# Optimization experiments

Hardware: AMD Instinct MI355X
Metric: run time of the kernel (lower is better)

The kernel has to match this reference:

```python
import jax, jax.numpy as jnp
import numpy as np

N_QUBITS = 6
DIM = 2 ** N_QUBITS  # 64
Q_LAYERS = 2
CHUNK = 16

# ---- single-qubit rotation gate matrices (batched over leading dim) ----

def _rx(t):
    c = jnp.cos(t / 2).astype(jnp.complex64)
    s = jnp.sin(t / 2).astype(jnp.complex64)
    return jnp.stack([jnp.stack([c, -1j * s], -1), jnp.stack([-1j * s, c], -1)], -2)

def _ry(t):
    c = jnp.cos(t / 2).astype(jnp.complex64)
    s = jnp.sin(t / 2).astype(jnp.complex64)
    return jnp.stack([jnp.stack([c, -s], -1), jnp.stack([s, c], -1)], -2)

def _rz(t):
    e = jnp.exp(-0.5j * t.astype(jnp.complex64))
    z = jnp.zeros_like(e)
    return jnp.stack([jnp.stack([e, z], -1), jnp.stack([z, jnp.conj(e)], -1)], -2)


def _apply_1q(state, gate, wire):
    # state: (B, 64) complex64; gate: (B,2,2). PennyLane wire 0 = most-significant bit.
    dl, dr = 2 ** wire, 2 ** (N_QUBITS - 1 - wire)
    s = state.reshape(-1, dl, 2, dr)
    s = jnp.einsum('bkj,bljr->blkr', gate, s)
    return s.reshape(-1, DIM)


def _apply_crx(state, theta, control, target):
    s = state.reshape((-1,) + (2,) * N_QUBITS)
    s = jnp.moveaxis(s, (control + 1, target + 1), (1, 2))
    g = _rx(theta)  # (B,2,2)
    s1 = jnp.einsum('bkj,bj...->bk...', g, s[:, 1])
    s = jnp.concatenate([s[:, :1], s1[:, None]], axis=1)
    s = jnp.moveaxis(s, (1, 2), (control + 1, target + 1))
    return s.reshape(-1, DIM)


def _ansatz(state, params, n_layers):
    # unified ansatz: per layer, RX/RY/RZ on each qubit, ring of CRX forward, ring of CRX backward
    idx = 0
    for _ in range(n_layers):
        for i in range(N_QUBITS):
            state = _apply_1q(state, _rx(params[:, idx]), i)
            state = _apply_1q(state, _ry(params[:, idx + 1]), i)
            state = _apply_1q(state, _rz(params[:, idx + 2]), i)
            idx += 3
        for i in range(N_QUBITS):
            state = _apply_crx(state, params[:, idx], i, (i + 1) % N_QUBITS)
            idx += 1
        for i in range(N_QUBITS - 1, -1, -1):
            state = _apply_crx(state, params[:, idx], i, (i - 1) % N_QUBITS)
            idx += 1
    return state


_PX = jnp.array([[0, 1], [1, 0]], jnp.complex64)
_PY = jnp.array([[0, -1j], [1j, 0]], jnp.complex64)
_PZ = jnp.array([[1, 0], [0, -1]], jnp.complex64)


def _expvals(state):
    # expectations of X_i, Y_i, Z_i for all qubits -> (B, 3*n_qubits)
    outs = []
    B = state.shape[0]
    for P in (_PX, _PY, _PZ):
        g = jnp.broadcast_to(P, (B, 2, 2))
        for i in range(N_QUBITS):
            ps = _apply_1q(state, g, i)
            outs.append(jnp.sum(jnp.conj(state) * ps, axis=1).real)
    return jnp.stack(outs, axis=1).astype(jnp.float32)


def _forward(x, emb_w, emb_b, att_w1, att_b1, att_w2, att_b2, proj_w, proj_b,
             mix_re, mix_im, qff_params, out_w, out_b, ln_g, ln_b,
             cls_w1, cls_b1, cls_w2, cls_b2):
    B, C, T = x.shape
    # classical feature extractor: (B,C,T) -> (B,T,D)
    feats = jnp.einsum('bct,cd->btd', x, emb_w) + emb_b
    D = feats.shape[-1]
    n_chunks = T // CHUNK
    xc = feats.reshape(B, n_chunks, CHUNK, D)
    # attention-weighted chunk aggregation
    h = jnp.tanh(xc @ att_w1 + att_b1)
    scores = h @ att_w2 + att_b2                      # (B,nc,CHUNK,1)
    w = jax.nn.softmax(scores, axis=2)
    chunks = jnp.sum(w * xc, axis=2)                  # (B,nc,D)
    # quantum attention core: per-chunk ansatz params
    params = jax.nn.sigmoid(chunks @ proj_w + proj_b)  # (B,nc,60)
    flat = params.reshape(B * n_chunks, -1)
    state0 = jnp.zeros((B * n_chunks, DIM), jnp.complex64).at[:, 0].set(1.0)
    evolved = _ansatz(state0, flat, Q_LAYERS).reshape(B, n_chunks, DIM)
    # LCU mixing
    coeffs = (mix_re + 1j * mix_im).astype(jnp.complex64)
    coeffs = coeffs / (jnp.abs(coeffs).sum() + 1e-8)
    mixed = jnp.einsum('bti,t->bi', evolved, coeffs)
    norms = jnp.linalg.norm(mixed, axis=1, keepdims=True)
    mixed = mixed / (norms + 1e-9)
    # quantum feed-forward (shared params) + multi-observable measurement
    qp = jnp.broadcast_to(qff_params, (B, qff_params.shape[0]))
    qstate = _ansatz(mixed, qp, 1)
    qfeat = _expvals(qstate)                          # (B,18)
    out = qfeat @ out_w + out_b                       # (B,D)
    # LayerNorm
    mu = out.mean(-1, keepdims=True)
    var = out.var(-1, keepdims=True)
    out = (out - mu) / jnp.sqrt(var + 1e-5) * ln_g + ln_b
    # classifier head
    h2 = jax.nn.relu(out @ cls_w1 + cls_b1)
    return h2 @ cls_w2 + cls_b2


def setup_inputs() -> dict:
    key = jax.random.key(0)
    ks = jax.random.split(key, 20)
    B, C, T, D = 128, 64, 2048, 256
    NC = T // CHUNK        # 128 chunks
    NCP = 5 * N_QUBITS * Q_LAYERS  # 60 circuit params
    def nrm(k, shape, scale=0.05):
        return jax.random.normal(k, shape, jnp.float32) * scale
    return {
        'x': jax.random.normal(ks[0], (B, C, T), jnp.float32),
        'emb_w': nrm(ks[1], (C, D)), 'emb_b': nrm(ks[2], (D,)),
        'att_w1': nrm(ks[3], (D, D // 2)), 'att_b1': nrm(ks[4], (D // 2,)),
        'att_w2': nrm(ks[5], (D // 2, 1)), 'att_b2': nrm(ks[6], (1,)),
        'proj_w': nrm(ks[7], (D, NCP)), 'proj_b': nrm(ks[8], (NCP,)),
        'mix_re': jax.random.uniform(ks[9], (NC,), jnp.float32),
        'mix_im': jax.random.uniform(ks[10], (NC,), jnp.float32),
        'qff_params': nrm(ks[11], (5 * N_QUBITS,), 0.1),
        'out_w': nrm(ks[12], (3 * N_QUBITS, D)), 'out_b': nrm(ks[13], (D,)),
        'ln_g': jnp.ones((D,), jnp.float32), 'ln_b': jnp.zeros((D,), jnp.float32),
        'cls_w1': nrm(ks[14], (D, D)), 'cls_b1': nrm(ks[15], (D,)),
        'cls_w2': nrm(ks[16], (D, 2)), 'cls_b2': nrm(ks[17], (2,)),
    }


def reference(x, emb_w, emb_b, att_w1, att_b1, att_w2, att_b2, proj_w, proj_b,
              mix_re, mix_im, qff_params, out_w, out_b, ln_g, ln_b,
              cls_w1, cls_b1, cls_w2, cls_b2):
    return _forward(x, emb_w, emb_b, att_w1, att_b1, att_w2, att_b2, proj_w, proj_b,
                    mix_re, mix_im, qff_params, out_w, out_b, ln_g, ln_b,
                    cls_w1, cls_b1, cls_w2, cls_b2)
```

## Files before the change

### kernel.cpp

```cpp
#include <hip/hip_runtime.h>
#include <math.h>

#define NQ    6
#define QDIM  64
#define BB    128
#define CC    64
#define TT    2048
#define DD    256
#define NCH   128
#define CHLEN 16
#define HH    128
#define NCP   60

typedef __bf16 bf16x8 __attribute__((ext_vector_type(8)));
typedef float  f32x4  __attribute__((ext_vector_type(4)));

__device__ __forceinline__ unsigned short bfbits(__bf16 v) {
  return __builtin_bit_cast(unsigned short, v);
}

__device__ __forceinline__ float fast_tanh(float x) {
  float e = __expf(2.f * x);
  return 1.f - 2.f / (e + 1.f);
}

__device__ __forceinline__ float wave_sum(float v) {
#pragma unroll
  for (int off = 32; off >= 1; off >>= 1) v += __shfl_xor(v, off, 64);
  return v;
}

__device__ __forceinline__ void g_rx(float& re, float& im, int lane, int m, float half) {
  float c = __cosf(half), s = __sinf(half);
  float pre = __shfl_xor(re, m, 64);
  float pim = __shfl_xor(im, m, 64);
  float nre = c * re + s * pim;
  float nim = c * im - s * pre;
  re = nre; im = nim;
}
__device__ __forceinline__ void g_ry(float& re, float& im, int lane, int m, float half) {
  float c = __cosf(half), s = __sinf(half);
  float pre = __shfl_xor(re, m, 64);
  float pim = __shfl_xor(im, m, 64);
  float sg = (lane & m) ? s : -s;
  re = c * re + sg * pre;
  im = c * im + sg * pim;
}
__device__ __forceinline__ void g_rz(float& re, float& im, int lane, int m, float half) {
  float c = __cosf(half), s = __sinf(half);
  float sg = (lane & m) ? s : -s;
  float nre = c * re - sg * im;
  float nim = c * im + sg * re;
  re = nre; im = nim;
}
__device__ __forceinline__ void g_crx(float& re, float& im, int lane, int mc, int mt, float half) {
  float c = __cosf(half), s = __sinf(half);
  float pre = __shfl_xor(re, mt, 64);
  float pim = __shfl_xor(im, mt, 64);
  if (lane & mc) {
    float nre = c * re + s * pim;
    float nim = c * im - s * pre;
    re = nre; im = nim;
  }
}
__device__ __forceinline__ void ansatz_layer(float& re, float& im, int lane,
                                             const float* p) {
#pragma unroll
  for (int q = 0; q < 6; ++q) {
    int m = 1 << (5 - q);
    g_rx(re, im, lane, m, 0.5f * p[3 * q + 0]);
    g_ry(re, im, lane, m, 0.5f * p[3 * q + 1]);
    g_rz(re, im, lane, m, 0.5f * p[3 * q + 2]);
  }
#pragma unroll
  for (int q = 0; q < 6; ++q)
    g_crx(re, im, lane, 1 << (5 - q), 1 << (5 - ((q + 1) % 6)), 0.5f * p[18 + q]);
#pragma unroll
  for (int q = 5; q >= 0; --q)
    g_crx(re, im, lane, 1 << (5 - q), 1 << (5 - ((q + 5) % 6)), 0.5f * p[24 + (5 - q)]);
}

__global__ __launch_bounds__(256) void k0_prep(
    const float* __restrict__ emb_w, const float* __restrict__ emb_b,
    const float* __restrict__ att_w1, const float* __restrict__ att_b1,
    const float* __restrict__ proj_w, const float* __restrict__ proj_b,
    __bf16* __restrict__ WfH, __bf16* __restrict__ WfL,
    __bf16* __restrict__ PfH, __bf16* __restrict__ PfL,
    float* __restrict__ b_fused, float* __restrict__ pb_fused) {
  int idx = blockIdx.x * 256 + threadIdx.x;
  if (idx < 65536) {
    int out = idx >> 3, part = idx & 7;
    int j = out & 127, k = out >> 7;
    int d0 = part * 32;
    float a = 0.f;
#pragma unroll 8
    for (int d = d0; d < d0 + 32; ++d)
      a = fmaf(emb_w[k * 256 + d], att_w1[d * 128 + j], a);
    a += __shfl_xor(a, 1, 64); a += __shfl_xor(a, 2, 64); a += __shfl_xor(a, 4, 64);
    if (part == 0) {
      __bf16 h = (__bf16)a;
      WfH[j * 64 + k] = h; WfL[j * 64 + k] = (__bf16)(a - (float)h);
    }
  } else if (idx < 98304) {
    int i2 = idx - 65536;
    int out = i2 >> 3, part = i2 & 7;
    int n = out & 63, k = out >> 6;
    float a = 0.f;
    if (n < 60) {
      int d0 = part * 32;
#pragma unroll 8
      for (int d = d0; d < d0 + 32; ++d)
        a = fmaf(emb_w[k * 256 + d], proj_w[d * 60 + n], a);
    }
    a += __shfl_xor(a, 1, 64); a += __shfl_xor(a, 2, 64); a += __shfl_xor(a, 4, 64);
    if (part == 0) {
      __bf16 h = (__bf16)a;
      PfH[n * 64 + k] = h; PfL[n * 64 + k] = (__bf16)(a - (float)h);
    }
  } else if (idx < 99328) {
    int i3 = idx - 98304;
    int out = i3 >> 3, part = i3 & 7;
    float a = (part == 0) ? att_b1[out] : 0.f;
    int d0 = part * 32;
#pragma unroll 8
    for (int d = d0; d < d0 + 32; ++d)
      a = fmaf(emb_b[d], att_w1[d * 128 + out], a);
    a += __shfl_xor(a, 1, 64); a += __shfl_xor(a, 2, 64); a += __shfl_xor(a, 4, 64);
    if (part == 0) b_fused[out] = a;
  } else if (idx < 99840) {
    int i4 = idx - 99328;
    int out = i4 >> 3, part = i4 & 7;
    float a = 0.f;
    if (out < 60) {
      if (part == 0) a = proj_b[out];
      int d0 = part * 32;
#pragma unroll 8
      for (int d = d0; d < d0 + 32; ++d)
        a = fmaf(emb_b[d], proj_w[d * 60 + out], a);
    }
    a += __shfl_xor(a, 1, 64); a += __shfl_xor(a, 2, 64); a += __shfl_xor(a, 4, 64);
    if (part == 0) pb_fused[out] = a;
  }
}

__global__ __launch_bounds__(256, 8) void k1_fused(
    const float* __restrict__ x, const float* __restrict__ att_w2,
    const __bf16* __restrict__ WfH, const __bf16* __restrict__ WfL,
    const __bf16* __restrict__ PfH, const __bf16* __restrict__ PfL,
    const float* __restrict__ b_fused, const float* __restrict__ pb_fused,
    float2* __restrict__ evolved) {
  const int blk = blockIdx.x;
  const int b = blk >> 5, cq = blk & 31;
  const int tid = threadIdx.x, wv = tid >> 6, lane = tid & 63;
  const int l15 = lane & 15, quad = lane >> 4;

  __shared__ float4 uniF4[1024];
  __shared__ float scoreS[4][64];
  __shared__ float wSm[4][16];
  __shared__ __align__(16) __bf16 axH[4][64];
  __shared__ __align__(16) __bf16 axL[4][64];
  char* uni = (char*)uniF4;
  bf16x8* afH = (bf16x8*)uni;
  bf16x8* afL = (bf16x8*)(uni + 8192);
  float*  paramsS = (float*)uni;
  float4* matS    = (float4*)(uni + 960);
  float2* crxS    = (float2*)(uni + 4032);

  {
    unsigned short* afHu = (unsigned short*)uni;
    unsigned short* afLu = (unsigned short*)(uni + 8192);
#pragma unroll
    for (int p = 0; p < 2; ++p) {
      int slot = p * 256 + tid;
      int t4 = slot & 15, kp = slot >> 4;
      int k0 = kp * 2;
      const float* base = x + ((size_t)(b * 64 + k0)) * 2048 + cq * 64 + t4 * 4;
      float4 v0 = *(const float4*)base;
      float4 v1 = *(const float4*)(base + 2048);
      int ks = k0 >> 5, colq = (k0 >> 3) & 3, e = k0 & 7;
      float a0[4] = {v0.x, v0.y, v0.z, v0.w};
      float a1[4] = {v1.x, v1.y, v1.z, v1.w};
#pragma unroll
      for (int dt = 0; dt < 4; ++dt) {
        int t = t4 * 4 + dt;
        int frag = (t >> 4) * 2 + ks;
        int ln = (t & 15) + colq * 16;
        int widx = frag * 512 + ln * 8 + e;
        __bf16 h0 = (__bf16)a0[dt]; __bf16 l0 = (__bf16)(a0[dt] - (float)h0);
        __bf16 h1 = (__bf16)a1[dt]; __bf16 l1 = (__bf16)(a1[dt] - (float)h1);
        *(ushort2*)(afHu + widx) = make_ushort2(bfbits(h0), bfbits(h1));
        *(ushort2*)(afLu + widx) = make_ushort2(bfbits(l0), bfbits(l1));
      }
    }
  }
  __syncthreads();

  {
    float w2v[2], b1v[2];
#pragma unroll
    for (int jt = 0; jt < 2; ++jt) {
      int j = wv * 32 + jt * 16 + l15;
      w2v[jt] = att_w2[j];
      b1v[jt] = b_fused[j];
    }
#pragma unroll
    for (int half = 0; half < 2; ++half) {
      f32x4 acc[2][2];
#pragma unroll
      for (int a2 = 0; a2 < 2; ++a2)
#pragma unroll
        for (int c2 = 0; c2 < 2; ++c2) acc[a2][c2] = (f32x4){0.f, 0.f, 0.f, 0.f};
#pragma unroll
      for (int ks = 0; ks < 2; ++ks)
#pragma unroll
        for (int jt = 0; jt < 2; ++jt) {
          const size_t row = (size_t)(wv * 32 + jt * 16 + l15) * 64 + ks * 32 + 8 * quad;
          bf16x8 bh = *(const bf16x8*)(WfH + row);
          bf16x8 bl = *(const bf16x8*)(WfL + row);
#pragma unroll
          for (int mtl = 0; mtl < 2; ++mtl) {
            int frag = (half * 2 + mtl) * 2 + ks;
            bf16x8 ah = afH[frag * 64 + lane];
            bf16x8 al = afL[frag * 64 + lane];
            acc[mtl][jt] = __builtin_amdgcn_mfma_f32_16x16x32_bf16(ah, bh, acc[mtl][jt], 0, 0, 0);
            acc[mtl][jt] = __builtin_amdgcn_mfma_f32_16x16x32_bf16(al, bh, acc[mtl][jt], 0, 0, 0);
            acc[mtl][jt] = __builtin_amdgcn_mfma_f32_16x16x32_bf16(ah, bl, acc[mtl][jt], 0, 0, 0);
          }
        }
#pragma unroll
      for (int mtl = 0; mtl < 2; ++mtl)
#pragma unroll
        for (int r = 0; r < 4; ++r) {
          float sc = fast_tanh(acc[mtl][0][r] + b1v[0]) * w2v[0] +
                     fast_tanh(acc[mtl][1][r] + b1v[1]) * w2v[1];
          sc += __shfl_xor(sc, 1, 64);
          sc += __shfl_xor(sc, 2, 64);
          sc += __shfl_xor(sc, 4, 64);
          sc += __shfl_xor(sc, 8, 64);
          if (l15 == 0) scoreS[wv][(half * 2 + mtl) * 16 + quad * 4 + r] = sc;
        }
    }
  }
  __syncthreads();

  if (tid < 64) {
    const int c = tid >> 4, t = tid & 15, ct = c * 16 + t;
    float s = (scoreS[0][ct] + scoreS[1][ct]) + (scoreS[2][ct] + scoreS[3][ct]);
    float mx = s;
    mx = fmaxf(mx, __shfl_xor(mx, 1, 64));
    mx = fmaxf(mx, __shfl_xor(mx, 2, 64));
    mx = fmaxf(mx, __shfl_xor(mx, 4, 64));
    mx = fmaxf(mx, __shfl_xor(mx, 8, 64));
    float e = __expf(s - mx);
    float sum = e;
    sum += __shfl_xor(sum, 1, 64);
    sum += __shfl_xor(sum, 2, 64);
    sum += __shfl_xor(sum, 4, 64);
    sum += __shfl_xor(sum, 8, 64);
    wSm[c][t] = e / sum;
  }
  __syncthreads();

  {
    float wgt = wSm[wv][l15];
#pragma unroll
    for (int ks = 0; ks < 2; ++ks) {
      bf16x8 h8 = afH[(wv * 2 + ks) * 64 + lane];
      bf16x8 l8 = afL[(wv * 2 + ks) * 64 + lane];
      float part[8];
#pragma unroll
      for (int e = 0; e < 8; ++e) part[e] = wgt * ((float)h8[e] + (float)l8[e]);
#pragma unroll
      for (int off = 1; off <= 8; off <<= 1)
#pragma unroll
        for (int e = 0; e < 8; ++e) part[e] += __shfl_xor(part[e], off, 64);
      int kbase = ks * 32 + quad * 8;
      if (l15 == 0) {
        bf16x8 H;
#pragma unroll
        for (int e = 0; e < 8; ++e) H[e] = (__bf16)part[e];
        *(bf16x8*)(&axH[wv][kbase]) = H;
      } else if (l15 == 1) {
        bf16x8 L;
#pragma unroll
        for (int e = 0; e < 8; ++e) {
          __bf16 hh = (__bf16)part[e];
          L[e] = (__bf16)(part[e] - (float)hh);
        }
        *(bf16x8*)(&axL[wv][kbase]) = L;
      }
    }
  }
  __syncthreads();

  {
    const int jout = wv * 16 + l15;
    f32x4 acc3 = (f32x4){0.f, 0.f, 0.f, 0.f};
#pragma unroll
    for (int ks = 0; ks < 2; ++ks) {
      const size_t row = (size_t)jout * 64 + ks * 32 + 8 * quad;
      bf16x8 bh = *(const bf16x8*)(PfH + row);
      bf16x8 bl = *(const bf16x8*)(PfL + row);
      bf16x8 ax = (bf16x8)(__bf16)0.f, alx = (bf16x8)(__bf16)0.f;
      if (l15 < 4) {
        ax  = *(const bf16x8*)(&axH[0][0] + l15 * 64 + ks * 32 + 8 * quad);
        alx = *(const bf16x8*)(&axL[0][0] + l15 * 64 + ks * 32 + 8 * quad);
      }
      acc3 = __builtin_amdgcn_mfma_f32_16x16x32_bf16(ax, bh, acc3, 0, 0, 0);
      acc3 = __builtin_amdgcn_mfma_f32_16x16x32_bf16(alx, bh, acc3, 0, 0, 0);
      acc3 = __builtin_amdgcn_mfma_f32_16x16x32_bf16(ax, bl, acc3, 0, 0, 0);
    }
    if (jout < 60 && quad == 0) {
      float pbias = pb_fused[jout];
      const int layer = (jout >= 30) ? 1 : 0;
      const int pm = jout - layer * 30;
#pragma unroll
      for (int r = 0; r < 4; ++r) {
        float a = acc3[r] + pbias;
        float p = 1.f / (1.f + __expf(-a));
        paramsS[r * 60 + jout] = p;
        if (pm >= 18) {
          float sn, cs;
          __sincosf(0.5f * p, &sn, &cs);
          crxS[r * 24 + layer * 12 + (pm - 18)] = make_float2(cs, sn);
        }
      }
    }
  }
  __syncthreads();

  if (tid < 48) {
    const int r = tid / 12, g = tid % 12;
    const float* pp = paramsS + r * 60 + (g / 6) * 30 + (g % 6) * 3;
    float sa, ca, sb, cb, sg, cg;
    __sincosf(0.5f * pp[0], &sa, &ca);
    __sincosf(0.5f * pp[1], &sb, &cb);
    __sincosf(0.5f * pp[2], &sg, &cg);
    float m00r = cb * ca, m00i = sb * sa;
    float m01r = -sb * ca, m01i = -cb * sa;
    float m10r = sb * ca, m10i = -cb * sa;
    float m11r = cb * ca, m11i = -sb * sa;
    float4 b0, b1;
    b0.x = cg * m00r + sg * m00i;  b0.y = cg * m00i - sg * m00r;
    b0.z = cg * m01r + sg * m01i;  b0.w = cg * m01i - sg * m01r;
    b1.x = cg * m11r - sg * m11i;  b1.y = cg * m11i + sg * m11r;
    b1.z = cg * m10r - sg * m10i;  b1.w = cg * m10i + sg * m10r;
    matS[(r * 12 + g) * 2 + 0] = b0;
    matS[(r * 12 + g) * 2 + 1] = b1;
  }
  __syncthreads();

  {
    float re = (lane == 0) ? 1.f : 0.f, im = 0.f;
    const float4* mats = matS + wv * 24;
    const float2* crxs = crxS + wv * 24;
#pragma unroll
    for (int l = 0; l < 2; ++l) {
#pragma unroll
      for (int q = 0; q < 6; ++q) {
        const int m = 1 << (5 - q);
        float4 M = mats[(l * 6 + q) * 2 + ((lane & m) ? 1 : 0)];
        float pre = __shfl_xor(re, m, 64);
        float pim = __shfl_xor(im, m, 64);
        float nre = M.x * re - M.y * im + M.z * pre - M.w * pim;
        float nim = M.x * im + M.y * re + M.z * pim + M.w * pre;
        re = nre; im = nim;
      }
#pragma unroll
      for (int e = 0; e < 12; ++e) {
        const int q = (e < 6) ? e : (11 - e);
        const int mc = 1 << (5 - q);
        const int mt = (e < 6) ? (1 << (5 - ((q + 1) % 6)))
                               : (1 << (5 - ((q + 5) % 6)));
        float2 cs = crxs[l * 12 + e];
        float pre = __shfl_xor(re, mt, 64);
        float pim = __shfl_xor(im, mt, 64);
        float nre = fmaf(cs.y, pim, cs.x * re);
        float nim = fmaf(-cs.y, pre, cs.x * im);
        bool act = (lane & mc) != 0;
        re = act ? nre : re;
        im = act ? nim : im;
      }
    }
    evolved[((size_t)b * NCH + cq * 4 + wv) * QDIM + lane] = make_float2(re, im);
  }
}

__global__ __launch_bounds__(512) void k3_head(
    const float2* __restrict__ evolved, const float* __restrict__ mix_re,
    const float* __restrict__ mix_im, const float* __restrict__ qff,
    const float* __restrict__ out_w, const float* __restrict__ out_b,
    const float* __restrict__ ln_g, const float* __restrict__ ln_b,
    const float* __restrict__ cls_w1, const float* __restrict__ cls_b1,
    const float* __restrict__ cls_w2, const float* __restrict__ cls_b2,
    float* __restrict__ outp) {
  const int b = blockIdx.x, tid = threadIdx.x, wv = tid >> 6, lane = tid & 63;
  __shared__ float mreS[8][64], mimS[8][64];
  __shared__ float qfeatS[18];
  __shared__ float outS[DD];
  __shared__ float redS[8];
  __shared__ float clsR[2][DD];

  float are = 0.f, aim = 0.f;
#pragma unroll 4
  for (int t = wv * 16; t < wv * 16 + 16; ++t) {
    float2 e = evolved[((size_t)b * NCH + t) * QDIM + lane];
    float cr = mix_re[t], ci = mix_im[t];
    are = fmaf(cr, e.x, are); are = fmaf(-ci, e.y, are);
    aim = fmaf(cr, e.y, aim); aim = fmaf(ci, e.x, aim);
  }
  mreS[wv][lane] = are; mimS[wv][lane] = aim;
  __syncthreads();

  if (wv == 0) {
    float r0 = mix_re[lane], i0 = mix_im[lane];
    float r1 = mix_re[lane + 64], i1 = mix_im[lane + 64];
    float sp = sqrtf(r0 * r0 + i0 * i0) + sqrtf(r1 * r1 + i1 * i1);
    float S = wave_sum(sp) + 1e-8f;
    float re = 0.f, im = 0.f;
#pragma unroll
    for (int w = 0; w < 8; ++w) { re += mreS[w][lane]; im += mimS[w][lane]; }
    float invS = 1.f / S;
    re *= invS; im *= invS;
    float n2 = wave_sum(re * re + im * im);
    float scl = 1.f / (sqrtf(n2) + 1e-9f);
    re *= scl; im *= scl;
    float qp[30];
#pragma unroll
    for (int i = 0; i < 30; ++i) qp[i] = qff[i];
    ansatz_layer(re, im, lane, qp);
#pragma unroll
    for (int q = 0; q < 6; ++q) {
      int m = 1 << (5 - q);
      float pre = __shfl_xor(re, m, 64), pim = __shfl_xor(im, m, 64);
      float vx = re * pre + im * pim;
      float vy = (lane & m) ? (im * pre - re * pim) : (re * pim - im * pre);
      float vz = (lane & m) ? -(re * re + im * im) : (re * re + im * im);
      vx = wave_sum(vx); vy = wave_sum(vy); vz = wave_sum(vz);
      if (lane == 0) { qfeatS[q] = vx; qfeatS[6 + q] = vy; qfeatS[12 + q] = vz; }
    }
  }
  __syncthreads();

  float o = 0.f, dv = 0.f;
  if (tid < 256) {
    o = out_b[tid];
#pragma unroll
    for (int k = 0; k < 18; ++k) o = fmaf(qfeatS[k], out_w[k * DD + tid], o);
    float s1 = wave_sum(o);
    if (lane == 0) redS[wv] = s1;
  }
  __syncthreads();
  float mu = (redS[0] + redS[1] + redS[2] + redS[3]) * (1.f / 256.f);
  if (tid < 256) {
    dv = o - mu;
    float s2 = wave_sum(dv * dv);
    if (lane == 0) redS[wv] = s2;
  }
  __syncthreads();
  float var = (redS[0] + redS[1] + redS[2] + redS[3]) * (1.f / 256.f);
  if (tid < 256) {
    outS[tid] = dv / sqrtf(var + 1e-5f) * ln_g[tid] + ln_b[tid];
  }
  __syncthreads();

  {
    const int dd = tid & 255, hh = tid >> 8;
    float r = (hh == 0) ? cls_b1[dd] : 0.f;
#pragma unroll 8
    for (int d = hh * 128; d < hh * 128 + 128; ++d)
      r = fmaf(outS[d], cls_w1[(size_t)d * DD + dd], r);
    clsR[hh][dd] = r;
  }
  __syncthreads();
  if (tid < 256) {
    float r = fmaxf(clsR[0][tid] + clsR[1][tid], 0.f);
    float p0 = wave_sum(r * cls_w2[tid * 2 + 0]);
    float p1 = wave_sum(r * cls_w2[tid * 2 + 1]);
    if (lane == 0) { mreS[0][wv] = p0; mreS[1][wv] = p1; }
  }
  __syncthreads();
  if (tid == 0) {
    outp[b * 2 + 0] = (mreS[0][0] + mreS[0][1]) + (mreS[0][2] + mreS[0][3]) + cls_b2[0];
    outp[b * 2 + 1] = (mreS[1][0] + mreS[1][1]) + (mreS[1][2] + mreS[1][3]) + cls_b2[1];
  }
}

extern "C" void kernel_launch(void* const* d_in, const int* in_sizes, int n_in,
                              void* d_out, int out_size, void* d_ws, size_t ws_size,
                              hipStream_t stream) {
  const float* x      = (const float*)d_in[0];
  const float* emb_w  = (const float*)d_in[1];
  const float* emb_b  = (const float*)d_in[2];
  const float* att_w1 = (const float*)d_in[3];
  const float* att_b1 = (const float*)d_in[4];
  const float* att_w2 = (const float*)d_in[5];
  const float* proj_w = (const float*)d_in[7];
  const float* proj_b = (const float*)d_in[8];
  const float* mix_re = (const float*)d_in[9];
  const float* mix_im = (const float*)d_in[10];
  const float* qff    = (const float*)d_in[11];
  const float* out_w  = (const float*)d_in[12];
  const float* out_b  = (const float*)d_in[13];
  const float* ln_g   = (const float*)d_in[14];
  const float* ln_b   = (const float*)d_in[15];
  const float* cls_w1 = (const float*)d_in[16];
  const float* cls_b1 = (const float*)d_in[17];
  const float* cls_w2 = (const float*)d_in[18];
  const float* cls_b2 = (const float*)d_in[19];

  char* ws = (char*)d_ws;
  float2* evolved = (float2*)ws;
  size_t off = 8388608;
  __bf16* WfH = (__bf16*)(ws + off); off += 16384;
  __bf16* WfL = (__bf16*)(ws + off); off += 16384;
  __bf16* PfH = (__bf16*)(ws + off); off += 8192;
  __bf16* PfL = (__bf16*)(ws + off); off += 8192;
  float* b_fused  = (float*)(ws + off); off += 512;
  float* pb_fused = (float*)(ws + off); off += 256;

  k0_prep<<<390, 256, 0, stream>>>(emb_w, emb_b, att_w1, att_b1, proj_w, proj_b,
                                   WfH, WfL, PfH, PfL, b_fused, pb_fused);
  k1_fused<<<BB * 32, 256, 0, stream>>>(
      x, att_w2, WfH, WfL, PfH, PfL, b_fused, pb_fused, evolved);
  k3_head<<<BB, 512, 0, stream>>>(evolved, mix_re, mix_im, qff, out_w, out_b,
                                  ln_g, ln_b, cls_w1, cls_b1, cls_w2, cls_b2,
                                  (float*)d_out);
}
```

Measured before the change: 209.0 us.

## Project per-timestep features before attention pooling to drop a reduce stage

The projection matrix is now applied to every timestep's features inside the attention GEMM loop, reusing the same A fragments. The softmax weights are then applied to the projected outputs with a small shuffle reduction. This reorders the linear algebra (pool then project becomes project then pool) and removes the weighted-sum shuffle pass, the axH/axL shared buffers and one barrier, at the cost of extra MFMAs and more accumulator registers. The launch-bounds occupancy hint of 8 is also dropped.

```diff
diff --git a/kernel.cpp b/kernel.cpp
--- a/kernel.cpp
+++ b/kernel.cpp
@@ -143,7 +143,7 @@
   }
 }
 
-__global__ __launch_bounds__(256, 8) void k1_fused(
+__global__ __launch_bounds__(256) void k1_fused(
     const float* __restrict__ x, const float* __restrict__ att_w2,
     const __bf16* __restrict__ WfH, const __bf16* __restrict__ WfL,
     const __bf16* __restrict__ PfH, const __bf16* __restrict__ PfL,
@@ -156,9 +156,7 @@
 
   __shared__ float4 uniF4[1024];
   __shared__ float scoreS[4][64];
-  __shared__ float wSm[4][16];
-  __shared__ __align__(16) __bf16 axH[4][64];
-  __shared__ __align__(16) __bf16 axL[4][64];
+  __shared__ __align__(16) float wSm[4][16];
   char* uni = (char*)uniF4;
   bf16x8* afH = (bf16x8*)uni;
   bf16x8* afL = (bf16x8*)(uni + 8192);
@@ -195,7 +193,17 @@
   }
   __syncthreads();
 
+  f32x4 accp[4];
+#pragma unroll
+  for (int c = 0; c < 4; ++c) accp[c] = (f32x4){0.f, 0.f, 0.f, 0.f};
   {
+    const size_t prow = (size_t)(wv * 16 + l15) * 64 + 8 * quad;
+    bf16x8 pbh[2], pbl[2];
+#pragma unroll
+    for (int ks = 0; ks < 2; ++ks) {
+      pbh[ks] = *(const bf16x8*)(PfH + prow + ks * 32);
+      pbl[ks] = *(const bf16x8*)(PfL + prow + ks * 32);
+    }
     float w2v[2], b1v[2];
 #pragma unroll
     for (int jt = 0; jt < 2; ++jt) {
@@ -211,7 +219,14 @@
 #pragma unroll
         for (int c2 = 0; c2 < 2; ++c2) acc[a2][c2] = (f32x4){0.f, 0.f, 0.f, 0.f};
 #pragma unroll
-      for (int ks = 0; ks < 2; ++ks)
+      for (int ks = 0; ks < 2; ++ks) {
+        bf16x8 ah[2], al[2];
+#pragma unroll
+        for (int mtl = 0; mtl < 2; ++mtl) {
+          int frag = (half * 2 + mtl) * 2 + ks;
+          ah[mtl] = afH[frag * 64 + lane];
+          al[mtl] = afL[frag * 64 + lane];
+        }
 #pragma unroll
         for (int jt = 0; jt < 2; ++jt) {
           const size_t row = (size_t)(wv * 32 + jt * 16 + l15) * 64 + ks * 32 + 8 * quad;
@@ -219,14 +234,19 @@
           bf16x8 bl = *(const bf16x8*)(WfL + row);
 #pragma unroll
           for (int mtl = 0; mtl < 2; ++mtl) {
-            int frag = (half * 2 + mtl) * 2 + ks;
-            bf16x8 ah = afH[frag * 64 + lane];
-            bf16x8 al = afL[frag * 64 + lane];
-            acc[mtl][jt] = __builtin_amdgcn_mfma_f32_16x16x32_bf16(ah, bh, acc[mtl][jt], 0, 0, 0);
-            acc[mtl][jt] = __builtin_amdgcn_mfma_f32_16x16x32_bf16(al, bh, acc[mtl][jt], 0, 0, 0);
-            acc[mtl][jt] = __builtin_amdgcn_mfma_f32_16x16x32_bf16(ah, bl, acc[mtl][jt], 0, 0, 0);
+            acc[mtl][jt] = __builtin_amdgcn_mfma_f32_16x16x32_bf16(ah[mtl], bh, acc[mtl][jt], 0, 0, 0);
+            acc[mtl][jt] = __builtin_amdgcn_mfma_f32_16x16x32_bf16(al[mtl], bh, acc[mtl][jt], 0, 0, 0);
+            acc[mtl][jt] = __builtin_amdgcn_mfma_f32_16x16x32_bf16(ah[mtl], bl, acc[mtl][jt], 0, 0, 0);
           }
         }
+#pragma unroll
+        for (int mtl = 0; mtl < 2; ++mtl) {
+          int c = half * 2 + mtl;
+          accp[c] = __builtin_amdgcn_mfma_f32_16x16x32_bf16(ah[mtl], pbh[ks], accp[c], 0, 0, 0);
+          accp[c] = __builtin_amdgcn_mfma_f32_16x16x32_bf16(al[mtl], pbh[ks], accp[c], 0, 0, 0);
+          accp[c] = __builtin_amdgcn_mfma_f32_16x16x32_bf16(ah[mtl], pbl[ks], accp[c], 0, 0, 0);
+        }
+      }
 #pragma unroll
       for (int mtl = 0; mtl < 2; ++mtl)
 #pragma unroll
@@ -262,67 +282,30 @@
   __syncthreads();
 
   {
-    float wgt = wSm[wv][l15];
-#pragma unroll
-    for (int ks = 0; ks < 2; ++ks) {
-      bf16x8 h8 = afH[(wv * 2 + ks) * 64 + lane];
-      bf16x8 l8 = afL[(wv * 2 + ks) * 64 + lane];
-      float part[8];
-#pragma unroll
-      for (int e = 0; e < 8; ++e) part[e] = wgt * ((float)h8[e] + (float)l8[e]);
-#pragma unroll
-      for (int off = 1; off <= 8; off <<= 1)
-#pragma unroll
-        for (int e = 0; e < 8; ++e) part[e] += __shfl_xor(part[e], off, 64);
-      int kbase = ks * 32 + quad * 8;
-      if (l15 == 0) {
-        bf16x8 H;
-#pragma unroll
-        for (int e = 0; e < 8; ++e) H[e] = (__bf16)part[e];
-        *(bf16x8*)(&axH[wv][kbase]) = H;
-      } else if (l15 == 1) {
-        bf16x8 L;
-#pragma unroll
-        for (int e = 0; e < 8; ++e) {
-          __bf16 hh = (__bf16)part[e];
-          L[e] = (__bf16)(part[e] - (float)hh);
-        }
-        *(bf16x8*)(&axL[wv][kbase]) = L;
-      }
-    }
-  }
-  __syncthreads();
-
-  {
-    const int jout = wv * 16 + l15;
-    f32x4 acc3 = (f32x4){0.f, 0.f, 0.f, 0.f};
-#pragma unroll
-    for (int ks = 0; ks < 2; ++ks) {
-      const size_t row = (size_t)jout * 64 + ks * 32 + 8 * quad;
-      bf16x8 bh = *(const bf16x8*)(PfH + row);
-      bf16x8 bl = *(const bf16x8*)(PfL + row);
-      bf16x8 ax = (bf16x8)(__bf16)0.f, alx = (bf16x8)(__bf16)0.f;
-      if (l15 < 4) {
-        ax  = *(const bf16x8*)(&axH[0][0] + l15 * 64 + ks * 32 + 8 * quad);
-        alx = *(const bf16x8*)(&axL[0][0] + l15 * 64 + ks * 32 + 8 * quad);
-      }
-      acc3 = __builtin_amdgcn_mfma_f32_16x16x32_bf16(ax, bh, acc3, 0, 0, 0);
-      acc3 = __builtin_amdgcn_mfma_f32_16x16x32_bf16(alx, bh, acc3, 0, 0, 0);
-      acc3 = __builtin_amdgcn_mfma_f32_16x16x32_bf16(ax, bl, acc3, 0, 0, 0);
-    }
-    if (jout < 60 && quad == 0) {
-      float pbias = pb_fused[jout];
-      const int layer = (jout >= 30) ? 1 : 0;
-      const int pm = jout - layer * 30;
-#pragma unroll
-      for (int r = 0; r < 4; ++r) {
-        float a = acc3[r] + pbias;
+    float v[4];
+#pragma unroll
+    for (int c = 0; c < 4; ++c) {
+      float4 wq = *(const float4*)&wSm[c][quad * 4];
+      float a = wq.x * accp[c][0] + wq.y * accp[c][1] +
+                wq.z * accp[c][2] + wq.w * accp[c][3];
+      a += __shfl_xor(a, 16, 64);
+      a += __shfl_xor(a, 32, 64);
+      v[c] = a;
+    }
+    const int n = wv * 16 + l15;
+    if (quad == 0 && n < 60) {
+      float pbias = pb_fused[n];
+      const int layer = (n >= 30) ? 1 : 0;
+      const int pm = n - layer * 30;
+#pragma unroll
+      for (int c = 0; c < 4; ++c) {
+        float a = v[c] + pbias;
         float p = 1.f / (1.f + __expf(-a));
-        paramsS[r * 60 + jout] = p;
+        paramsS[c * 60 + n] = p;
         if (pm >= 18) {
           float sn, cs;
           __sincosf(0.5f * p, &sn, &cs);
-          crxS[r * 24 + layer * 12 + (pm - 18)] = make_float2(cs, sn);
+          crxS[c * 24 + layer * 12 + (pm - 18)] = make_float2(cs, sn);
         }
       }
     }
```

After: 205.7 us. About the same (-1.6%).
